# Kernel tuning notes

Measured on AMD Instinct MI355X. Metric: run time of the kernel, lower is better.

The kernel has to match this reference:

```python
import jax, jax.numpy as jnp
import numpy as np

N_NODES = 50000
N_EDGES = 600000
IN_CH = 128
HID_CH = 128
OUT_CH = 64
NUM_GRAPHS = 512


def _gcn_conv(x, W, b, src, dst, n):
    # PyG GCNConv (eval): h = D^{-1/2} (A + I) D^{-1/2} (x W) + b
    h = x @ W  # [N, C]
    loop = jnp.arange(n)
    s = jnp.concatenate([src, loop])  # add self-loops
    d = jnp.concatenate([dst, loop])
    deg = jax.ops.segment_sum(jnp.ones_like(d, dtype=h.dtype), d, num_segments=n)
    dinv = jnp.where(deg > 0, jax.lax.rsqrt(deg), 0.0)
    coef = dinv[s] * dinv[d]  # [E+N]
    msg = h[s] * coef[:, None]  # gather + scale
    out = jax.ops.segment_sum(msg, d, num_segments=n)  # scatter-add
    return out + b


def setup_inputs() -> dict:
    key = jax.random.key(0)
    ks = jax.random.split(key, 10)
    x = jax.random.normal(ks[0], (N_NODES, IN_CH), dtype=jnp.float32)
    edge_index = jax.random.randint(ks[1], (2, N_EDGES), 0, N_NODES, dtype=jnp.int64)
    batch = jnp.sort(jax.random.randint(ks[2], (N_NODES,), 0, NUM_GRAPHS, dtype=jnp.int64))
    sc1 = 1.0 / np.sqrt(IN_CH)
    sc2 = 1.0 / np.sqrt(HID_CH)
    W1 = jax.random.uniform(ks[3], (IN_CH, HID_CH), jnp.float32, -sc1, sc1)
    b1 = jnp.zeros((HID_CH,), jnp.float32)
    W2 = jax.random.uniform(ks[4], (HID_CH, HID_CH), jnp.float32, -sc2, sc2)
    b2 = jnp.zeros((HID_CH,), jnp.float32)
    Wlin = jax.random.uniform(ks[5], (HID_CH, OUT_CH), jnp.float32, -sc2, sc2)
    blin = jax.random.uniform(ks[6], (OUT_CH,), jnp.float32, -sc2, sc2)
    return {"x": x, "W1": W1, "b1": b1, "W2": W2, "b2": b2,
            "Wlin": Wlin, "blin": blin, "edge_index": edge_index, "batch": batch}


def reference(x, W1, b1, W2, b2, Wlin, blin, edge_index, batch):
    n = x.shape[0]
    src, dst = edge_index[0], edge_index[1]
    h = jax.nn.relu(_gcn_conv(x, W1, b1, src, dst, n))
    # dropout: identity in eval mode (training=False)
    h = jax.nn.relu(_gcn_conv(h, W2, b2, src, dst, n))
    # global mean pool over graphs
    summed = jax.ops.segment_sum(h, batch, num_segments=NUM_GRAPHS)
    cnt = jax.ops.segment_sum(jnp.ones((n,), h.dtype), batch, num_segments=NUM_GRAPHS)
    pooled = summed / jnp.maximum(cnt, 1.0)[:, None]
    return pooled @ Wlin + blin  # [NUM_GRAPHS, OUT_CH]
```

## Files before the change

### kernel.cpp

```cpp
#include <hip/hip_runtime.h>

#define N_NODES 50000
#define N_EDGES 600000
#define CH 128
#define NUM_GRAPHS 512
#define OUT_CH 64
#define DSH 6
#define DSTRIDE 64
#define CSH 4

typedef unsigned int uint32;
typedef __attribute__((ext_vector_type(8))) short short8;
typedef __attribute__((ext_vector_type(4))) float floatx4;

__device__ __forceinline__ uint32 bfpack(float a, float b) {
    uint32 ua = __builtin_bit_cast(uint32, a);
    uint32 ub = __builtin_bit_cast(uint32, b);
    ua = (ua + 0x7fffu + ((ua >> 16) & 1u)) >> 16;
    ub = (ub + 0x7fffu + ((ub >> 16) & 1u)) >> 16;
    return (ub << 16) | ua;
}
__device__ __forceinline__ unsigned short bfr(float f) {
    uint32 u = __builtin_bit_cast(uint32, f);
    u = (u + 0x7fffu + ((u >> 16) & 1u)) >> 16;
    return (unsigned short)u;
}
__device__ __forceinline__ float bf_lo(uint32 v) {
    return __builtin_bit_cast(float, v << 16);
}
__device__ __forceinline__ float bf_hi(uint32 v) {
    return __builtin_bit_cast(float, v & 0xffff0000u);
}

__global__ void k_prep(const float* __restrict__ W1, const float* __restrict__ W2,
                       unsigned short* __restrict__ W1t, unsigned short* __restrict__ W2t,
                       int* __restrict__ cur) {
    int idx = blockIdx.x * 256 + threadIdx.x;
    if (idx < (N_NODES << CSH)) cur[idx] = 0;
    if (idx < 32768) {
        int mat = idx >> 14;
        int rem = idx & 16383;
        int k = rem >> 7, c = rem & 127;
        const float* W = mat ? W2 : W1;
        unsigned short* Wt = mat ? W2t : W1t;
        Wt[c * 128 + k] = bfr(W[k * 128 + c]);
    }
}

__global__ void k_fill_pad(const int* __restrict__ src, const int* __restrict__ dst,
                           int* __restrict__ cur, int* __restrict__ srcs) {
    int e = blockIdx.x * 256 + threadIdx.x;
    if (e < N_EDGES) {
        int s = src[e];
        int d = dst[e];
        int p = atomicAdd(&cur[d << CSH], 1);
        srcs[(d << DSH) + p] = s;
    }
}

template <bool AF32>
__global__ __launch_bounds__(256, 2) void k_gemm(const void* __restrict__ Av,
                                                 const unsigned short* __restrict__ Wt,
                                                 const int* __restrict__ cur,
                                                 unsigned short* __restrict__ outb) {
    __shared__ __align__(16) unsigned short as_[128][136];
    __shared__ __align__(16) unsigned short bs[128][136];
    int tid = threadIdx.x;
    int row0 = blockIdx.x * 128;

    #pragma unroll
    for (int it = 0; it < 8; ++it) {
        int idx = it * 256 + tid;
        int r = idx >> 4, seg = idx & 15;
        int gr = min(row0 + r, N_NODES - 1);
        if (AF32) {
            const float4* ap = (const float4*)((const float*)Av + (size_t)gr * 128 + seg * 8);
            float4 v0 = ap[0], v1 = ap[1];
            uint4 pk;
            pk.x = bfpack(v0.x, v0.y); pk.y = bfpack(v0.z, v0.w);
            pk.z = bfpack(v1.x, v1.y); pk.w = bfpack(v1.z, v1.w);
            *(uint4*)&as_[r][seg * 8] = pk;
        } else {
            *(uint4*)&as_[r][seg * 8] =
                *(const uint4*)((const unsigned short*)Av + (size_t)gr * 128 + seg * 8);
        }
    }
    #pragma unroll
    for (int it = 0; it < 8; ++it) {
        int idx = it * 256 + tid;
        int c = idx >> 4, seg = idx & 15;
        *(uint4*)&bs[c][seg * 8] = *(const uint4*)&Wt[c * 128 + seg * 8];
    }
    __syncthreads();

    int w = tid >> 6, lane = tid & 63, q = lane >> 4, m = lane & 15;
    int q8 = q * 8;
    floatx4 acc[2][8];
    #pragma unroll
    for (int rt = 0; rt < 2; ++rt)
        #pragma unroll
        for (int ct = 0; ct < 8; ++ct) {
            floatx4 z = {0.f, 0.f, 0.f, 0.f};
            acc[rt][ct] = z;
        }

    #pragma unroll
    for (int kc = 0; kc < 128; kc += 32) {
        short8 a0 = *(const short8*)&as_[w * 32 + m][kc + q8];
        short8 a1 = *(const short8*)&as_[w * 32 + 16 + m][kc + q8];
        #pragma unroll
        for (int ct = 0; ct < 8; ++ct) {
            short8 b = *(const short8*)&bs[ct * 16 + m][kc + q8];
            acc[0][ct] = __builtin_amdgcn_mfma_f32_16x16x32_bf16(a0, b, acc[0][ct], 0, 0, 0);
            acc[1][ct] = __builtin_amdgcn_mfma_f32_16x16x32_bf16(a1, b, acc[1][ct], 0, 0, 0);
        }
    }

    #pragma unroll
    for (int rt = 0; rt < 2; ++rt) {
        #pragma unroll
        for (int i = 0; i < 4; ++i) {
            int gr = row0 + w * 32 + rt * 16 + q * 4 + i;
            if (gr < N_NODES) {
                float sc = rsqrtf((float)(cur[gr << CSH] + 1));
                #pragma unroll
                for (int ct = 0; ct < 8; ++ct) {
                    outb[(size_t)gr * 128 + ct * 16 + m] = bfr(acc[rt][ct][i] * sc);
                }
            }
        }
    }
}

template <bool BF16OUT>
__global__ __launch_bounds__(256) void k_agg(const uint32* __restrict__ hb,
                                             const int* __restrict__ cnt_arr,
                                             const int* __restrict__ srcs,
                                             const float* __restrict__ bias,
                                             void* __restrict__ outv) {
    int node = __builtin_amdgcn_readfirstlane(blockIdx.x * 4 + (threadIdx.x >> 6));
    int lane = threadIdx.x & 63;

    int cnt = cnt_arr[node << CSH];
    float dn = rsqrtf((float)(cnt + 1));
    uint32 vs = hb[node * 64 + lane];
    float ax = bf_lo(vs), ay = bf_hi(vs);

    int start = node << DSH;
    int last = start + cnt - 1;
    for (int j = 0; j < cnt; j += 8) {
        int i0 = start + j;
        int i1 = min(i0 + 1, last);
        int i2 = min(i0 + 2, last);
        int i3 = min(i0 + 3, last);
        int i4 = min(i0 + 4, last);
        int i5 = min(i0 + 5, last);
        int i6 = min(i0 + 6, last);
        int i7 = min(i0 + 7, last);
        int s0 = srcs[i0], s1 = srcs[i1], s2 = srcs[i2], s3 = srcs[i3];
        int s4 = srcs[i4], s5 = srcs[i5], s6 = srcs[i6], s7 = srcs[i7];
        uint32 v0 = hb[s0 * 64 + lane];
        uint32 v1 = hb[s1 * 64 + lane];
        uint32 v2 = hb[s2 * 64 + lane];
        uint32 v3 = hb[s3 * 64 + lane];
        uint32 v4 = hb[s4 * 64 + lane];
        uint32 v5 = hb[s5 * 64 + lane];
        uint32 v6 = hb[s6 * 64 + lane];
        uint32 v7 = hb[s7 * 64 + lane];
        int rem = cnt - j;
        v1 = (rem > 1) ? v1 : 0u;
        v2 = (rem > 2) ? v2 : 0u;
        v3 = (rem > 3) ? v3 : 0u;
        v4 = (rem > 4) ? v4 : 0u;
        v5 = (rem > 5) ? v5 : 0u;
        v6 = (rem > 6) ? v6 : 0u;
        v7 = (rem > 7) ? v7 : 0u;
        ax += bf_lo(v0); ay += bf_hi(v0);
        ax += bf_lo(v1); ay += bf_hi(v1);
        ax += bf_lo(v2); ay += bf_hi(v2);
        ax += bf_lo(v3); ay += bf_hi(v3);
        ax += bf_lo(v4); ay += bf_hi(v4);
        ax += bf_lo(v5); ay += bf_hi(v5);
        ax += bf_lo(v6); ay += bf_hi(v6);
        ax += bf_lo(v7); ay += bf_hi(v7);
    }
    float2 b = ((const float2*)bias)[lane];
    ax = fmaxf(ax * dn + b.x, 0.f);
    ay = fmaxf(ay * dn + b.y, 0.f);
    if (BF16OUT) ((uint32*)outv)[node * 64 + lane] = bfpack(ax, ay);
    else         ((float2*)outv)[node * 64 + lane] = make_float2(ax, ay);
}

__global__ __launch_bounds__(256) void k_pool_linear(const float* __restrict__ h,
                                                     const int* __restrict__ batch,
                                                     const float* __restrict__ Wl,
                                                     const float* __restrict__ bl,
                                                     float* __restrict__ out) {
    __shared__ int sb[2];
    __shared__ float4 sacc[256];
    __shared__ float xr[CH];
    __shared__ float po[4][OUT_CH];
    int g = blockIdx.x;
    int tid = threadIdx.x;
    if (tid < 2) {
        int target = g + tid;
        int lo = 0, hi = N_NODES;
        while (lo < hi) {
            int mid = (lo + hi) >> 1;
            if (batch[mid] < target) lo = mid + 1; else hi = mid;
        }
        sb[tid] = lo;
    }
    __syncthreads();
    int lo = sb[0], hi = sb[1];
    int q = tid & 31;
    int r = tid >> 5;
    const float4* h4 = (const float4*)h;
    float4 acc = make_float4(0.f, 0.f, 0.f, 0.f);
    for (int i = lo + r; i < hi; i += 8) {
        float4 v = h4[(size_t)i * 32 + q];
        acc.x += v.x; acc.y += v.y; acc.z += v.z; acc.w += v.w;
    }
    sacc[tid] = acc;
    __syncthreads();
    if (r == 0) {
        #pragma unroll
        for (int p = 1; p < 8; ++p) {
            float4 t = sacc[q + p * 32];
            acc.x += t.x; acc.y += t.y; acc.z += t.z; acc.w += t.w;
        }
        float inv = 1.f / (float)((hi - lo) > 0 ? (hi - lo) : 1);
        xr[q * 4 + 0] = acc.x * inv;
        xr[q * 4 + 1] = acc.y * inv;
        xr[q * 4 + 2] = acc.z * inv;
        xr[q * 4 + 3] = acc.w * inv;
    }
    __syncthreads();
    int c = tid & 63;
    int kh = tid >> 6;
    float o = 0.f;
    #pragma unroll 8
    for (int k = kh * 32; k < kh * 32 + 32; ++k) o += xr[k] * Wl[k * OUT_CH + c];
    po[kh][c] = o;
    __syncthreads();
    if (tid < OUT_CH) {
        float v = bl[tid] + po[0][tid] + po[1][tid] + po[2][tid] + po[3][tid];
        out[g * OUT_CH + tid] = v;
    }
}

extern "C" void kernel_launch(void* const* d_in, const int* in_sizes, int n_in,
                              void* d_out, int out_size, void* d_ws, size_t ws_size,
                              hipStream_t stream) {
    const float* x    = (const float*)d_in[0];
    const float* W1   = (const float*)d_in[1];
    const float* b1   = (const float*)d_in[2];
    const float* W2   = (const float*)d_in[3];
    const float* b2   = (const float*)d_in[4];
    const float* Wlin = (const float*)d_in[5];
    const float* blin = (const float*)d_in[6];
    const int* ei     = (const int*)d_in[7];
    const int* batch  = (const int*)d_in[8];
    const int* esrc = ei;
    const int* edst = ei + N_EDGES;
    float* out = (float*)d_out;

    char* w = (char*)d_ws;
    size_t o = 0;
    float* hA            = (float*)(w + o);          o += (size_t)N_NODES * CH * 4;
    unsigned short* hb   = (unsigned short*)(w + o); o += (size_t)N_NODES * CH * 2;
    uint32* habf         = (uint32*)(w + o);         o += (size_t)N_NODES * 64 * 4;
    unsigned short* W1t  = (unsigned short*)(w + o); o += 16384 * 2;
    unsigned short* W2t  = (unsigned short*)(w + o); o += 16384 * 2;
    int* srcs            = (int*)(w + o);            o += (size_t)N_NODES * DSTRIDE * 4;
    int* cur             = (int*)(w + o);            o += (size_t)(N_NODES << CSH) * 4;
    (void)ws_size; (void)in_sizes; (void)n_in; (void)out_size;

    dim3 b256(256);
    k_prep<<<dim3(((N_NODES << CSH) + 255) / 256), b256, 0, stream>>>(W1, W2, W1t, W2t, cur);
    k_fill_pad<<<dim3((N_EDGES + 255) / 256), b256, 0, stream>>>(esrc, edst, cur, srcs);

    dim3 gG((N_NODES + 127) / 128);
    dim3 gA(N_NODES / 4);
    k_gemm<true><<<gG, b256, 0, stream>>>(x, W1t, cur, hb);
    k_agg<true><<<gA, b256, 0, stream>>>((const uint32*)hb, cur, srcs, b1, habf);
    k_gemm<false><<<gG, b256, 0, stream>>>(habf, W2t, cur, hb);
    k_agg<false><<<gA, b256, 0, stream>>>((const uint32*)hb, cur, srcs, b2, hA);
    k_pool_linear<<<dim3(NUM_GRAPHS), b256, 0, stream>>>(hA, batch, Wlin, blin, out);
}
```

Before: 204.8 us.

## Replace per-node atomic edge fill with two-level bucket then LDS bin fill

Edge placement now happens in two passes. First, edges are bucketed into 782 coarse buckets of 64 destination nodes using one global atomic per bucket, with source and local destination packed into one word. Then each block bins its bucket in LDS and writes the padded per-node source lists and compact counts with coalesced stores. This replaces the scattered per-node atomics and the zeroing of a large padded counter array. In exchange it adds a kernel launch and an intermediate buffer, and it caps each bucket at 1024 edges and each node at 64, which could drop edges if the degree distribution is skewed.

```diff
diff --git a/kernel.cpp b/kernel.cpp
--- a/kernel.cpp
+++ b/kernel.cpp
@@ -7,7 +7,8 @@
 #define OUT_CH 64
 #define DSH 6
 #define DSTRIDE 64
-#define CSH 4
+#define NBUCK 782
+#define BPAD 1024
 
 typedef unsigned int uint32;
 typedef __attribute__((ext_vector_type(8))) short short8;
@@ -34,9 +35,9 @@
 
 __global__ void k_prep(const float* __restrict__ W1, const float* __restrict__ W2,
                        unsigned short* __restrict__ W1t, unsigned short* __restrict__ W2t,
-                       int* __restrict__ cur) {
+                       int* __restrict__ ccnt) {
     int idx = blockIdx.x * 256 + threadIdx.x;
-    if (idx < (N_NODES << CSH)) cur[idx] = 0;
+    if (idx < NBUCK * 16) ccnt[idx] = 0;
     if (idx < 32768) {
         int mat = idx >> 14;
         int rem = idx & 16383;
@@ -47,15 +48,45 @@
     }
 }
 
-__global__ void k_fill_pad(const int* __restrict__ src, const int* __restrict__ dst,
-                           int* __restrict__ cur, int* __restrict__ srcs) {
+__global__ void k_bucket(const int* __restrict__ src, const int* __restrict__ dst,
+                         int* __restrict__ ccnt, uint32* __restrict__ cbuck) {
     int e = blockIdx.x * 256 + threadIdx.x;
     if (e < N_EDGES) {
         int s = src[e];
         int d = dst[e];
-        int p = atomicAdd(&cur[d << CSH], 1);
-        srcs[(d << DSH) + p] = s;
-    }
+        int b = d >> DSH;
+        int p = atomicAdd(&ccnt[b * 16], 1);
+        if (p < BPAD) cbuck[b * BPAD + p] = ((uint32)s << DSH) | (uint32)(d & (DSTRIDE - 1));
+    }
+}
+
+__global__ __launch_bounds__(256) void k_binfill(const int* __restrict__ ccnt,
+                                                 const uint32* __restrict__ cbuck,
+                                                 int* __restrict__ srcs,
+                                                 int* __restrict__ cur) {
+    __shared__ int lbin[DSTRIDE * 64];
+    __shared__ int lcnt[64];
+    int b = blockIdx.x;
+    int tid = threadIdx.x;
+    if (tid < 64) lcnt[tid] = 0;
+    __syncthreads();
+    int n = min(ccnt[b * 16], BPAD);
+    int node0 = b << DSH;
+    for (int i = tid; i < n; i += 256) {
+        uint32 v = cbuck[b * BPAD + i];
+        int dl = (int)(v & (DSTRIDE - 1));
+        int s = (int)(v >> DSH);
+        int p = atomicAdd(&lcnt[dl], 1);
+        if (p < DSTRIDE) lbin[dl * DSTRIDE + p] = s;
+    }
+    __syncthreads();
+    #pragma unroll
+    for (int it = 0; it < 16; ++it) {
+        int idx = it * 256 + tid;
+        int dl = idx >> DSH;
+        if (node0 + dl < N_NODES) srcs[(node0 << DSH) + idx] = lbin[idx];
+    }
+    if (tid < 64 && node0 + tid < N_NODES) cur[node0 + tid] = min(lcnt[tid], DSTRIDE);
 }
 
 template <bool AF32>
@@ -122,7 +153,7 @@
         for (int i = 0; i < 4; ++i) {
             int gr = row0 + w * 32 + rt * 16 + q * 4 + i;
             if (gr < N_NODES) {
-                float sc = rsqrtf((float)(cur[gr << CSH] + 1));
+                float sc = rsqrtf((float)(cur[gr] + 1));
                 #pragma unroll
                 for (int ct = 0; ct < 8; ++ct) {
                     outb[(size_t)gr * 128 + ct * 16 + m] = bfr(acc[rt][ct][i] * sc);
@@ -141,7 +172,7 @@
     int node = __builtin_amdgcn_readfirstlane(blockIdx.x * 4 + (threadIdx.x >> 6));
     int lane = threadIdx.x & 63;
 
-    int cnt = cnt_arr[node << CSH];
+    int cnt = cnt_arr[node];
     float dn = rsqrtf((float)(cnt + 1));
     uint32 vs = hb[node * 64 + lane];
     float ax = bf_lo(vs), ay = bf_hi(vs);
@@ -273,12 +304,15 @@
     unsigned short* W1t  = (unsigned short*)(w + o); o += 16384 * 2;
     unsigned short* W2t  = (unsigned short*)(w + o); o += 16384 * 2;
     int* srcs            = (int*)(w + o);            o += (size_t)N_NODES * DSTRIDE * 4;
-    int* cur             = (int*)(w + o);            o += (size_t)(N_NODES << CSH) * 4;
+    int* cur             = (int*)(w + o);            o += (size_t)N_NODES * 4;
+    int* ccnt            = (int*)(w + o);            o += (size_t)NBUCK * 16 * 4;
+    uint32* cbuck        = (uint32*)(w + o);         o += (size_t)NBUCK * BPAD * 4;
     (void)ws_size; (void)in_sizes; (void)n_in; (void)out_size;
 
     dim3 b256(256);
-    k_prep<<<dim3(((N_NODES << CSH) + 255) / 256), b256, 0, stream>>>(W1, W2, W1t, W2t, cur);
-    k_fill_pad<<<dim3((N_EDGES + 255) / 256), b256, 0, stream>>>(esrc, edst, cur, srcs);
+    k_prep<<<dim3(128), b256, 0, stream>>>(W1, W2, W1t, W2t, ccnt);
+    k_bucket<<<dim3((N_EDGES + 255) / 256), b256, 0, stream>>>(esrc, edst, ccnt, cbuck);
+    k_binfill<<<dim3(NBUCK), b256, 0, stream>>>(ccnt, cbuck, srcs, cur);
 
     dim3 gG((N_NODES + 127) / 128);
     dim3 gA(N_NODES / 4);
```

After: 205.7 us, median of 2. Within noise of the previous version (+0.5%).
